# Kernel tuning notes

Measured on AMD Instinct MI355X. Metric: run time of the kernel, lower is better.

Reference implementation:

```python
import jax, jax.numpy as jnp
import numpy as np

JOINTS = 17
SKELETON = ((1, 2), (0, 1), (0, 2), (2, 4), (1, 3), (6, 8), (8, 10), (5, 7), (7, 9),
            (12, 14), (14, 16), (11, 13), (13, 15), (5, 6), (11, 12), (5, 11), (6, 12),
            (3, 5), (4, 6))
DIM = 512
HEADS = 8
HEAD_DIM = DIM // HEADS
SCALE = HEAD_DIM ** -0.5
ON = 64           # obj_emb seq len; HEADS*ON must equal 512 (size of W)
HIDDEN = 4 * DIM
BN_EPS = 1e-5
LN_EPS = 1e-5


def make_adj():
    a = np.eye(JOINTS, dtype=np.float32)
    for i, j in SKELETON:
        a[i, j] = 1.0
        a[j, i] = 1.0
    return jnp.asarray(a)


def layer_norm(x, w, b):
    mu = jnp.mean(x, axis=-1, keepdims=True)
    var = jnp.var(x, axis=-1, keepdims=True)
    return (x - mu) * jax.lax.rsqrt(var + LN_EPS) * w + b


def setup_inputs() -> dict:
    key = jax.random.key(0)
    ks = jax.random.split(key, 12)
    B = 2048
    inp = {
        "noise": jax.random.normal(ks[0], (B, JOINTS, DIM), jnp.float32),
        "obj_emb": jax.random.normal(ks[1], (B, ON, DIM), jnp.float32),
        "ln1_w": jnp.ones((DIM,), jnp.float32),
        "ln1_b": jnp.zeros((DIM,), jnp.float32),
        "ln2_w": jnp.ones((DIM,), jnp.float32),
        "ln2_b": jnp.zeros((DIM,), jnp.float32),
        "q_w": jax.random.normal(ks[2], (DIM, DIM), jnp.float32) * 0.02,
        "kv_w": jax.random.normal(ks[3], (2 * DIM, DIM), jnp.float32) * 0.02,
        "W": jax.random.normal(ks[4], (HEADS * ON, HEADS * ON), jnp.float32) * 0.001,
        "bn_g": jnp.ones((HEADS * ON,), jnp.float32),
        "bn_b": jnp.zeros((HEADS * ON,), jnp.float32),
        "proj_w": jax.random.normal(ks[5], (DIM, DIM), jnp.float32) * 0.02,
        "proj_b": jnp.zeros((DIM,), jnp.float32),
        "fc1_w": jax.random.normal(ks[6], (HIDDEN, DIM), jnp.float32) * 0.02,
        "fc1_b": jnp.zeros((HIDDEN,), jnp.float32),
        "fc2_w": jax.random.normal(ks[7], (DIM, HIDDEN), jnp.float32) * 0.02,
        "fc2_b": jnp.zeros((DIM,), jnp.float32),
    }
    return inp


def reference(noise, obj_emb, ln1_w, ln1_b, ln2_w, ln2_b, q_w, kv_w, W,
              bn_g, bn_b, proj_w, proj_b, fc1_w, fc1_b, fc2_w, fc2_b):
    B = noise.shape[0]
    adj = make_adj()

    # --- attention branch (norm1 applied to both inputs with same params) ---
    x1 = layer_norm(noise, ln1_w, ln1_b)          # [B,17,C]
    e1 = layer_norm(obj_emb, ln1_w, ln1_b)        # [B,64,C]

    q = (x1 @ q_w.T).reshape(B, JOINTS, HEADS, HEAD_DIM).transpose(0, 2, 1, 3)  # [B,H,17,hd]
    kv = (e1 @ kv_w.T).reshape(B, ON, 2, HEADS, HEAD_DIM).transpose(2, 0, 3, 1, 4)
    k, v = kv[0], kv[1]                            # [B,H,64,hd]

    attn = jnp.einsum('bhnd,bhmd->bhnm', q, k) * SCALE        # [B,H,17,64]
    attn = attn.transpose(0, 2, 1, 3).reshape(B, JOINTS, HEADS * ON)  # [B,17,512]
    attn = attn @ W                                            # [B,17,512]

    # BatchNorm1d (training mode): stats over B*17 rows, biased variance
    flat = attn.reshape(B * JOINTS, HEADS * ON)
    mu = jnp.mean(flat, axis=0)
    var = jnp.var(flat, axis=0)
    flat = (flat - mu) * jax.lax.rsqrt(var + BN_EPS) * bn_g + bn_b
    attn = flat.reshape(B, JOINTS, HEADS * ON)

    attn = jnp.einsum('ij,bjk->bik', adj, attn)               # adjacency bmm
    attn = attn.reshape(B, JOINTS, HEADS, ON).transpose(0, 2, 1, 3)  # [B,H,17,64]
    attn = jax.nn.softmax(attn, axis=-1)

    x = jnp.einsum('bhnm,bhmd->bhnd', attn, v)                # [B,H,17,hd]
    x = x.transpose(0, 2, 1, 3).reshape(B, JOINTS, DIM)
    x = x @ proj_w.T + proj_b

    x = noise + x

    # --- MLP branch ---
    y = layer_norm(x, ln2_w, ln2_b)
    y = jax.nn.gelu(y @ fc1_w.T + fc1_b, approximate=False)
    y = y @ fc2_w.T + fc2_b
    return x + y
```

## Files before the change

### kernel.cpp

```cpp
#include <hip/hip_runtime.h>
#include <math.h>

typedef unsigned short ushort_t;
typedef short short8 __attribute__((ext_vector_type(8)));
typedef float f32x4 __attribute__((ext_vector_type(4)));

#define MFMA16(a,b,c) __builtin_amdgcn_mfma_f32_16x16x32_bf16(a,b,c,0,0,0)

__device__ __forceinline__ ushort_t f2bf(float f){
  unsigned u = __builtin_bit_cast(unsigned, f);
  u += 0x7fffu + ((u >> 16) & 1u);
  return (ushort_t)(u >> 16);
}

__device__ __forceinline__ void gld16(const void* g, void* l){
  __builtin_amdgcn_global_load_lds(
      (const __attribute__((address_space(1))) void*)g,
      (__attribute__((address_space(3))) void*)l, 16, 0, 0);
}

__global__ __launch_bounds__(256)
void prep_weights(const float* __restrict__ q_w, const float* __restrict__ kv_w,
                  const float* __restrict__ proj_w, const float* __restrict__ fc1_w,
                  const float* __restrict__ fc2_w, const float* __restrict__ Wm,
                  const float* __restrict__ ln1w, const float* __restrict__ ln2w,
                  ushort_t* __restrict__ q_wb, ushort_t* __restrict__ kv_wb,
                  ushort_t* __restrict__ proj_wb, ushort_t* __restrict__ fc1_wb,
                  ushort_t* __restrict__ fc2_wb, ushort_t* __restrict__ Wt_b)
{
  int i = blockIdx.x*256 + threadIdx.x;
  if (i < 262144){
    q_wb[i] = f2bf(q_w[i] * ln1w[i & 511]);
  } else if (i < 786432){
    int j = i - 262144;
    kv_wb[j] = f2bf(kv_w[j] * ln1w[j & 511]);
  } else if (i < 1048576){
    int j = i - 786432;
    proj_wb[j] = f2bf(proj_w[j]);
  } else if (i < 2097152){
    int j = i - 1048576;
    fc1_wb[j] = f2bf(fc1_w[j] * ln2w[j & 511]);
  } else if (i < 3145728){
    int j = i - 2097152;
    fc2_wb[j] = f2bf(fc2_w[j]);
  } else if (i < 3407872){
    int j = i - 3145728;
    int n = j >> 9, k = j & 511;
    Wt_b[j] = f2bf(Wm[(k << 9) + n]);
  }
}

__global__ __launch_bounds__(64)
void prep_bias(const float* __restrict__ q_w, const float* __restrict__ kv_w,
               const float* __restrict__ fc1_w, const float* __restrict__ ln1b,
               const float* __restrict__ ln2b, const float* __restrict__ fc1_b,
               float* __restrict__ qbias, float* __restrict__ kvbias,
               float* __restrict__ fc1bias)
{
  int blk = blockIdx.x, lane = threadIdx.x;
  const float* w; const float* lnb; float* o; float base = 0.f; int n;
  if (blk < 512){ n = blk; w = q_w; lnb = ln1b; o = qbias; }
  else if (blk < 1536){ n = blk - 512; w = kv_w; lnb = ln1b; o = kvbias; }
  else { n = blk - 1536; w = fc1_w; lnb = ln2b; o = fc1bias; }
  float s = 0.f;
  for (int k = lane; k < 512; k += 64) s += w[(size_t)n*512 + k]*lnb[k];
  for (int m = 32; m; m >>= 1) s += __shfl_xor(s, m);
  if (lane == 0){
    if (blk >= 1536) base = fc1_b[n];
    o[n] = s + base;
  }
}

__global__ __launch_bounds__(256)
void lnorm(const float* __restrict__ X, ushort_t* __restrict__ O){
  int row = blockIdx.x*4 + (threadIdx.x >> 6);
  int lane = threadIdx.x & 63;
  const float4* p = (const float4*)(X + (size_t)row*512 + lane*8);
  float4 a = p[0], c = p[1];
  float s = a.x+a.y+a.z+a.w + c.x+c.y+c.z+c.w;
  float q = a.x*a.x+a.y*a.y+a.z*a.z+a.w*a.w + c.x*c.x+c.y*c.y+c.z*c.z+c.w*c.w;
  for (int m = 32; m; m >>= 1){ s += __shfl_xor(s, m); q += __shfl_xor(q, m); }
  float mn = s*(1.f/512.f);
  float rs = rsqrtf(q*(1.f/512.f) - mn*mn + 1e-5f);
  short8 pk;
  pk[0]=(short)f2bf((a.x-mn)*rs); pk[1]=(short)f2bf((a.y-mn)*rs);
  pk[2]=(short)f2bf((a.z-mn)*rs); pk[3]=(short)f2bf((a.w-mn)*rs);
  pk[4]=(short)f2bf((c.x-mn)*rs); pk[5]=(short)f2bf((c.y-mn)*rs);
  pk[6]=(short)f2bf((c.z-mn)*rs); pk[7]=(short)f2bf((c.w-mn)*rs);
  *(short8*)(O + (size_t)row*512 + lane*8) = pk;
}

template<int BN, int EPI>
__global__ __launch_bounds__(512, 4)
void gemm256(const ushort_t* __restrict__ A, const ushort_t* __restrict__ Bt,
             int M, int N, int K,
             const float* __restrict__ bias, const float* __restrict__ resid,
             void* __restrict__ out, void* __restrict__ out2)
{
  constexpr int NR    = BN / 64;
  constexpr int ASLOT = 256 * 32;
  constexpr int BSLOT = BN * 32;
  constexpr int SLOT  = ASLOT + BSLOT;
  __shared__ __align__(16) ushort_t lds[3 * SLOT];

  const int tid  = threadIdx.x;
  const int wave = tid >> 6, lane = tid & 63;
  const int wm   = wave >> 2, wn = wave & 3;
  const int l15  = lane & 15, lq = lane >> 4;

  const int nwg = gridDim.x;
  const int qc = nwg >> 3, rc = nwg & 7;
  const int xcd = blockIdx.x & 7, sl = blockIdx.x >> 3;
  const int bid = (xcd < rc ? xcd*(qc+1) : rc*(qc+1) + (xcd-rc)*qc) + sl;

  const int tiles_n = N / BN;
  const int tn = bid % tiles_n, tm = bid / tiles_n;
  const int tileM = tm * 256, tileN = tn * BN;

  const int gsw = (((tid & 3) - ((tid >> 3) & 3)) & 3) * 8;
  const int srow = tid >> 2;

  int offA[8], offB[NR];
#pragma unroll
  for (int mi = 0; mi < 8; mi++){
    int r = wm*128 + mi*16 + l15;
    offA[mi] = r*32 + (((lq + (r >> 1)) & 3) * 8);
  }
#pragma unroll
  for (int ni = 0; ni < NR; ni++){
    int r = wn*(BN/4) + ni*16 + l15;
    offB[ni] = ASLOT + r*32 + (((lq + (r >> 1)) & 3) * 8);
  }

  f32x4 acc[8][NR] = {};

  const int NT = K >> 5;

  auto stage = [&](int step, int slot){
    ushort_t* base = lds + slot * SLOT;
    const int k0 = step * 32 + gsw;
#pragma unroll
    for (int i = 0; i < 2; i++)
      gld16(A + (size_t)(tileM + i*128 + srow)*K + k0,
            base + i*4096 + wave*512);
#pragma unroll
    for (int i = 0; i < BN/128; i++)
      gld16(Bt + (size_t)(tileN + i*128 + srow)*K + k0,
            base + ASLOT + i*4096 + wave*512);
  };

  stage(0, 0);
  stage(1, 1);
  if constexpr (BN == 256) asm volatile("s_waitcnt vmcnt(4)" ::: "memory");
  else                     asm volatile("s_waitcnt vmcnt(3)" ::: "memory");
  __builtin_amdgcn_sched_barrier(0);
  __builtin_amdgcn_s_barrier();

  int rs = 0;
  for (int s = 0; s < NT; ++s){
    const ushort_t* sb = lds + rs * SLOT;
    short8 bfr[NR];
#pragma unroll
    for (int ni = 0; ni < NR; ni++)
      bfr[ni] = *(const short8*)(sb + offB[ni]);

    const bool more = (s + 2 < NT);
    if (more){
      int r2 = rs + 2; if (r2 >= 3) r2 -= 3;
      stage(s + 2, r2);
    }

    __builtin_amdgcn_s_setprio(1);
#pragma unroll
    for (int mi = 0; mi < 8; mi++){
      short8 af = *(const short8*)(sb + offA[mi]);
#pragma unroll
      for (int ni = 0; ni < NR; ni++)
        acc[mi][ni] = MFMA16(af, bfr[ni], acc[mi][ni]);
    }
    __builtin_amdgcn_s_setprio(0);

    if (more){
      if constexpr (BN == 256) asm volatile("s_waitcnt vmcnt(4)" ::: "memory");
      else                     asm volatile("s_waitcnt vmcnt(3)" ::: "memory");
    } else {
      asm volatile("s_waitcnt vmcnt(0)" ::: "memory");
    }
    __builtin_amdgcn_sched_barrier(0);
    __builtin_amdgcn_s_barrier();

    rs = (rs == 2) ? 0 : rs + 1;
  }

#pragma unroll
  for (int ni = 0; ni < NR; ni++){
    int col = tileN + wn*(BN/4) + ni*16 + l15;
    float bv = bias ? bias[col] : 0.f;
    float cs = 0.f, cq = 0.f;
#pragma unroll
    for (int mi = 0; mi < 8; mi++){
      f32x4 v = acc[mi][ni];
      int row0 = tileM + wm*128 + mi*16 + lq*4;
      if constexpr (EPI == 4){
        if (col < 512){
          for (int j = 0; j < 4; j++){
            size_t idx = (size_t)(row0 + j)*512 + col;
            ((ushort_t*)out)[idx] = f2bf(v[j] + bv);
          }
        } else {
          int hh = (col - 512) >> 6, dd = (col - 512) & 63;
          int bb = row0 >> 6, mm0 = row0 & 63;
          ushort_t pk[4];
          for (int j = 0; j < 4; j++) pk[j] = f2bf(v[j] + bv);
          *(uint2*)((ushort_t*)out2 + ((((size_t)bb*8 + hh)*64 + dd) << 6) + mm0) =
              *(const uint2*)pk;
        }
      } else {
        for (int j = 0; j < 4; j++){
          int row = row0 + j;
          size_t idx = (size_t)row*N + col;
          float x = v[j] + bv;
          if constexpr (EPI == 0) ((ushort_t*)out)[idx] = f2bf(x);
          else if constexpr (EPI == 1) ((float*)out)[idx] = x;
          else if constexpr (EPI == 2) ((float*)out)[idx] = x + resid[idx];
          else if constexpr (EPI == 3){
            float g = 0.5f*x*(1.f + erff(x*0.70710678118f));
            ((ushort_t*)out)[idx] = f2bf(g);
          }
          else if constexpr (EPI == 5){
            ((float*)out)[idx] = x;
            cs += x; cq += x*x;
          }
        }
      }
    }
    if constexpr (EPI == 5){
      cs += __shfl_xor(cs, 16); cs += __shfl_xor(cs, 32);
      cq += __shfl_xor(cq, 16); cq += __shfl_xor(cq, 32);
      if (lq == 0){
        float* sums = (float*)out2;
        atomicAdd(&sums[col], cs);
        atomicAdd(&sums[512 + col], cq);
      }
    }
  }
}

__global__ __launch_bounds__(256)
void qk_kernel(const ushort_t* __restrict__ Q, const ushort_t* __restrict__ Kb,
               ushort_t* __restrict__ S)
{
  int b = blockIdx.x;
  int wave = threadIdx.x >> 6, lane = threadIdx.x & 63;
  for (int h = wave; h < 8; h += 4){
    f32x4 acc[2][4] = {};
    for (int kk = 0; kk < 2; kk++){
      int kd = kk*32 + (lane >> 4)*8;
      short8 a[2], bb[4];
      for (int mi = 0; mi < 2; mi++){
        int n = mi*16 + (lane & 15); if (n > 16) n = 16;
        a[mi] = *(const short8*)&Q[((size_t)b*17 + n)*512 + h*64 + kd];
      }
      for (int ni = 0; ni < 4; ni++){
        int m = ni*16 + (lane & 15);
        bb[ni] = *(const short8*)&Kb[((size_t)b*64 + m)*512 + h*64 + kd];
      }
      for (int mi = 0; mi < 2; mi++)
        for (int ni = 0; ni < 4; ni++)
          acc[mi][ni] = MFMA16(a[mi], bb[ni], acc[mi][ni]);
    }
    for (int mi = 0; mi < 2; mi++)
      for (int ni = 0; ni < 4; ni++)
        for (int j = 0; j < 4; j++){
          int rr = mi*16 + (lane >> 4)*4 + j;
          if (rr < 17)
            S[((size_t)b*17 + rr)*512 + h*64 + ni*16 + (lane & 15)] =
                f2bf(acc[mi][ni][j]*0.125f);
        }
  }
}

__global__ __launch_bounds__(256)
void pv_kernel(const ushort_t* __restrict__ P, const ushort_t* __restrict__ Vt,
               ushort_t* __restrict__ X)
{
  int b = blockIdx.x;
  int wave = threadIdx.x >> 6, lane = threadIdx.x & 63;
  for (int h = wave; h < 8; h += 4){
    f32x4 acc[2][4] = {};
    for (int kk = 0; kk < 2; kk++){
      int km = kk*32 + (lane >> 4)*8;
      short8 a[2], bb[4];
      for (int mi = 0; mi < 2; mi++){
        int n = mi*16 + (lane & 15); if (n > 16) n = 16;
        a[mi] = *(const short8*)&P[((size_t)b*17 + n)*512 + h*64 + km];
      }
      for (int ni = 0; ni < 4; ni++){
        int d = ni*16 + (lane & 15);
        bb[ni] = *(const short8*)&Vt[(((size_t)b*8 + h)*64 + d)*64 + km];
      }
      for (int mi = 0; mi < 2; mi++)
        for (int ni = 0; ni < 4; ni++)
          acc[mi][ni] = MFMA16(a[mi], bb[ni], acc[mi][ni]);
    }
    for (int mi = 0; mi < 2; mi++)
      for (int ni = 0; ni < 4; ni++)
        for (int j = 0; j < 4; j++){
          int rr = mi*16 + (lane >> 4)*4 + j;
          if (rr < 17)
            X[((size_t)b*17 + rr)*512 + h*64 + ni*16 + (lane & 15)] =
                f2bf(acc[mi][ni][j]);
        }
  }
}

__global__ void bn_finalize(const float* __restrict__ sums, const float* __restrict__ g,
                            const float* __restrict__ b, float* __restrict__ scale,
                            float* __restrict__ shift, float invN){
  int c = blockIdx.x*256 + threadIdx.x;
  if (c < 512){
    float mean = sums[c]*invN;
    float var  = sums[512 + c]*invN - mean*mean;
    float sc = g[c]*rsqrtf(var + 1e-5f);
    scale[c] = sc; shift[c] = b[c] - mean*sc;
  }
}

__constant__ unsigned ADJM[17] = {
  0x7u, 0xFu, 0x17u, 0x2Au, 0x54u, 0x8E8u, 0x1170u, 0x2A0u, 0x540u,
  0x280u, 0x500u, 0x3820u, 0x5840u, 0xA800u, 0x15000u, 0xA000u, 0x14000u };

__global__ __launch_bounds__(256)
void bn_adj_softmax(const float* __restrict__ preBN, const float* __restrict__ scale,
                    const float* __restrict__ shift, ushort_t* __restrict__ Asm)
{
  __shared__ float yt[17*512];
  int b = blockIdx.x, tid = threadIdx.x;
  const float* src = preBN + (size_t)b*17*512;
  for (int i = tid; i < 17*512; i += 256){
    int c = i & 511;
    yt[i] = src[i]*scale[c] + shift[c];
  }
  __syncthreads();
  int qw = tid >> 4, l16 = tid & 15;
  for (int g = qw; g < 136; g += 16){
    int n = g >> 3, h = g & 7;
    float z[4];
    unsigned msk = ADJM[n];
    for (int u = 0; u < 4; u++){
      int c = h*64 + l16 + u*16;
      float sv = 0.f;
      unsigned mm = msk;
      while (mm){ int j = __ffs(mm) - 1; mm &= mm - 1; sv += yt[j*512 + c]; }
      z[u] = sv;
    }
    float mx = fmaxf(fmaxf(z[0], z[1]), fmaxf(z[2], z[3]));
    for (int m = 8; m; m >>= 1) mx = fmaxf(mx, __shfl_xor(mx, m, 16));
    float e0 = expf(z[0]-mx), e1 = expf(z[1]-mx), e2 = expf(z[2]-mx), e3 = expf(z[3]-mx);
    float ss = e0 + e1 + e2 + e3;
    for (int m = 8; m; m >>= 1) ss += __shfl_xor(ss, m, 16);
    float inv = 1.f/ss;
    size_t ob = ((size_t)b*17 + n)*512 + h*64 + l16;
    Asm[ob]      = f2bf(e0*inv);
    Asm[ob + 16] = f2bf(e1*inv);
    Asm[ob + 32] = f2bf(e2*inv);
    Asm[ob + 48] = f2bf(e3*inv);
  }
}

extern "C" void kernel_launch(void* const* d_in, const int* in_sizes, int n_in,
                              void* d_out, int out_size, void* d_ws, size_t ws_size,
                              hipStream_t stream)
{
  const float* noise  = (const float*)d_in[0];
  const float* obj    = (const float*)d_in[1];
  const float* ln1w   = (const float*)d_in[2];
  const float* ln1b   = (const float*)d_in[3];
  const float* ln2w   = (const float*)d_in[4];
  const float* ln2b   = (const float*)d_in[5];
  const float* q_w    = (const float*)d_in[6];
  const float* kv_w   = (const float*)d_in[7];
  const float* Wm     = (const float*)d_in[8];
  const float* bn_g   = (const float*)d_in[9];
  const float* bn_b   = (const float*)d_in[10];
  const float* proj_w = (const float*)d_in[11];
  const float* proj_b = (const float*)d_in[12];
  const float* fc1_w  = (const float*)d_in[13];
  const float* fc1_b  = (const float*)d_in[14];
  const float* fc2_w  = (const float*)d_in[15];
  const float* fc2_b  = (const float*)d_in[16];

  const int B  = in_sizes[0] / (17*512);
  const int M  = B*17;
  const int MO = B*64;

  const size_t MiB = 1ull << 20;
  char* ws = (char*)d_ws;

  ushort_t* q_wb    = (ushort_t*)(ws + 0*MiB);
  ushort_t* kv_wb   = (ushort_t*)(ws + 1*MiB);
  ushort_t* proj_wb = (ushort_t*)(ws + 2*MiB);
  ushort_t* fc1_wb  = (ushort_t*)(ws + 3*MiB);
  ushort_t* fc2_wb  = (ushort_t*)(ws + 5*MiB);
  ushort_t* Wt_b    = (ushort_t*)(ws + 7*MiB);
  float* qbias   = (float*)(ws + 7*MiB + 600*1024);
  float* kvbias  = qbias + 1024;
  float* fc1bias = kvbias + 1024;
  float* bnsum   = fc1bias + 2048;
  float* bnscale = bnsum + 1024;
  float* bnshift = bnscale + 512;

  char* R1 = ws + 8*MiB;
  char* R2 = ws + 136*MiB;
  char* R3 = ws + 264*MiB;

  ushort_t* e1b  = (ushort_t*)R1;
  ushort_t* Kb   = (ushort_t*)R2;
  ushort_t* Vtb  = (ushort_t*)R3;
  ushort_t* x1b  = (ushort_t*)R1;
  ushort_t* Qb   = (ushort_t*)(R1 + 35*MiB);
  ushort_t* Sb   = (ushort_t*)(R1 + 70*MiB);
  ushort_t* Asm  = (ushort_t*)R1;
  ushort_t* PVo  = (ushort_t*)(R1 + 35*MiB);
  float*    preBN = (float*)R2;
  float*    xres  = (float*)R2;
  ushort_t* yb   = (ushort_t*)(R2 + 69*MiB);
  ushort_t* h1   = (ushort_t*)(R2 + 104*MiB);
  float*    outp = (float*)d_out;

  hipMemsetAsync(bnsum, 0, 1024*4, stream);
  prep_weights<<<dim3(3407872/256), 256, 0, stream>>>(
      q_w, kv_w, proj_w, fc1_w, fc2_w, Wm, ln1w, ln2w,
      q_wb, kv_wb, proj_wb, fc1_wb, fc2_wb, Wt_b);
  prep_bias<<<dim3(3584), 64, 0, stream>>>(
      q_w, kv_w, fc1_w, ln1b, ln2b, fc1_b, qbias, kvbias, fc1bias);

  lnorm<<<dim3(MO/4), 256, 0, stream>>>(obj, e1b);
  gemm256<128,4><<<dim3((MO/256)*(1024/128)), 512, 0, stream>>>(
      e1b, kv_wb, MO, 1024, 512, kvbias, nullptr, Kb, Vtb);
  lnorm<<<dim3(M/4), 256, 0, stream>>>(noise, x1b);
  gemm256<128,0><<<dim3((M/256)*(512/128)), 512, 0, stream>>>(
      x1b, q_wb, M, 512, 512, qbias, nullptr, Qb, nullptr);
  qk_kernel<<<dim3(B), 256, 0, stream>>>(Qb, Kb, Sb);
  gemm256<128,5><<<dim3((M/256)*(512/128)), 512, 0, stream>>>(
      Sb, Wt_b, M, 512, 512, nullptr, nullptr, preBN, bnsum);
  bn_finalize<<<dim3(2), 256, 0, stream>>>(bnsum, bn_g, bn_b, bnscale, bnshift, 1.f/(float)M);
  bn_adj_softmax<<<dim3(B), 256, 0, stream>>>(preBN, bnscale, bnshift, Asm);
  pv_kernel<<<dim3(B), 256, 0, stream>>>(Asm, Vtb, PVo);
  gemm256<128,2><<<dim3((M/256)*(512/128)), 512, 0, stream>>>(
      PVo, proj_wb, M, 512, 512, proj_b, noise, xres, nullptr);

  lnorm<<<dim3(M/4), 256, 0, stream>>>(xres, yb);
  gemm256<128,3><<<dim3((M/256)*(2048/128)), 512, 0, stream>>>(
      yb, fc1_wb, M, 2048, 512, fc1bias, nullptr, h1, nullptr);
  gemm256<128,2><<<dim3((M/256)*(512/128)), 512, 0, stream>>>(
      h1, fc2_wb, M, 512, 2048, fc2_b, xres, outp, nullptr);
}
```

Baseline: 928.5 us.

## Replace GEMM with 256x256-tile, K=64, four-phase ping-pong pipelined kernel

Swaps the 256xBN triple-buffered GEMM for a 256x256 tile kernel with a 64-wide K step and double-buffered LDS (128KB). Each K iteration is split into four MFMA phases whose LDS fragment loads are interleaved with partial global-to-LDS prefetches for later steps, using an 8-way XOR swizzle. The aim is more reuse per tile and better overlap of global loads with MFMA work. In exchange it lowers occupancy to 2 blocks per CU and launches half as many tiles, so the small-N GEMMs (N=512, M≈35k) get fewer workgroups to spread across CUs.

```diff
diff --git a/kernel.cpp b/kernel.cpp
--- a/kernel.cpp
+++ b/kernel.cpp
@@ -90,18 +90,14 @@
   *(short8*)(O + (size_t)row*512 + lane*8) = pk;
 }
 
-template<int BN, int EPI>
-__global__ __launch_bounds__(512, 4)
-void gemm256(const ushort_t* __restrict__ A, const ushort_t* __restrict__ Bt,
-             int M, int N, int K,
-             const float* __restrict__ bias, const float* __restrict__ resid,
-             void* __restrict__ out, void* __restrict__ out2)
-{
-  constexpr int NR    = BN / 64;
-  constexpr int ASLOT = 256 * 32;
-  constexpr int BSLOT = BN * 32;
-  constexpr int SLOT  = ASLOT + BSLOT;
-  __shared__ __align__(16) ushort_t lds[3 * SLOT];
+template<int EPI>
+__global__ __launch_bounds__(512, 2)
+void gemm8p(const ushort_t* __restrict__ A, const ushort_t* __restrict__ Bt,
+            int M, int N, int K,
+            const float* __restrict__ bias, const float* __restrict__ resid,
+            void* __restrict__ out, void* __restrict__ out2)
+{
+  __shared__ __align__(16) ushort_t lds[65536];
 
   const int tid  = threadIdx.x;
   const int wave = tid >> 6, lane = tid & 63;
@@ -113,94 +109,157 @@
   const int xcd = blockIdx.x & 7, sl = blockIdx.x >> 3;
   const int bid = (xcd < rc ? xcd*(qc+1) : rc*(qc+1) + (xcd-rc)*qc) + sl;
 
-  const int tiles_n = N / BN;
+  const int tiles_n = N >> 8;
   const int tn = bid % tiles_n, tm = bid / tiles_n;
-  const int tileM = tm * 256, tileN = tn * BN;
-
-  const int gsw = (((tid & 3) - ((tid >> 3) & 3)) & 3) * 8;
-  const int srow = tid >> 2;
-
-  int offA[8], offB[NR];
-#pragma unroll
-  for (int mi = 0; mi < 8; mi++){
-    int r = wm*128 + mi*16 + l15;
-    offA[mi] = r*32 + (((lq + (r >> 1)) & 3) * 8);
-  }
-#pragma unroll
-  for (int ni = 0; ni < NR; ni++){
-    int r = wn*(BN/4) + ni*16 + l15;
-    offB[ni] = ASLOT + r*32 + (((lq + (r >> 1)) & 3) * 8);
-  }
-
-  f32x4 acc[8][NR] = {};
-
-  const int NT = K >> 5;
-
-  auto stage = [&](int step, int slot){
-    ushort_t* base = lds + slot * SLOT;
-    const int k0 = step * 32 + gsw;
-#pragma unroll
-    for (int i = 0; i < 2; i++)
-      gld16(A + (size_t)(tileM + i*128 + srow)*K + k0,
-            base + i*4096 + wave*512);
-#pragma unroll
-    for (int i = 0; i < BN/128; i++)
-      gld16(Bt + (size_t)(tileN + i*128 + srow)*K + k0,
-            base + ASLOT + i*4096 + wave*512);
+  const int tileM = tm*256, tileN = tn*256;
+
+  const int srow = tid >> 3;
+  const int gsw  = (((tid & 7) - (srow & 7)) & 7) * 8;
+  const ushort_t* Agl = A  + (size_t)(tileM + srow)*K + gsw;
+  const ushort_t* Bgl = Bt + (size_t)(tileN + srow)*K + gsw;
+
+  auto stageA = [&](int kt, int buf, int h){
+    ushort_t* d = lds + buf*32768 + h*8192 + tid*8;
+    const ushort_t* s = Agl + (size_t)(h*128)*K + kt*64;
+    gld16(s, d);
+    gld16(s + (size_t)64*K, d + 4096);
   };
-
-  stage(0, 0);
-  stage(1, 1);
-  if constexpr (BN == 256) asm volatile("s_waitcnt vmcnt(4)" ::: "memory");
-  else                     asm volatile("s_waitcnt vmcnt(3)" ::: "memory");
+  auto stageB = [&](int kt, int buf, int h){
+    ushort_t* d = lds + buf*32768 + 16384 + h*8192 + tid*8;
+    const ushort_t* s = Bgl + (size_t)(h*128)*K + kt*64;
+    gld16(s, d);
+    gld16(s + (size_t)64*K, d + 4096);
+  };
+
+  const int rbase = l15 * 64;
+  const int sk0 = (((lq    ) + (l15 & 7)) & 7) * 8;
+  const int sk1 = (((lq + 4) + (l15 & 7)) & 7) * 8;
+
+  f32x4 acc[8][4] = {};
+  short8 aR[4][2], b0R[2][2], b1R[2][2];
+
+  auto ldA = [&](const ushort_t* bb, int qm){
+#pragma unroll
+    for (int i = 0; i < 4; i++){
+      int ro = ((qm*4 + i)*2 + wm)*1024 + rbase;
+      aR[i][0] = *(const short8*)(bb + ro + sk0);
+      aR[i][1] = *(const short8*)(bb + ro + sk1);
+    }
+  };
+  auto ldB0 = [&](const ushort_t* bb){
+#pragma unroll
+    for (int j = 0; j < 2; j++){
+      int ro = 16384 + (j*4 + wn)*1024 + rbase;
+      b0R[j][0] = *(const short8*)(bb + ro + sk0);
+      b0R[j][1] = *(const short8*)(bb + ro + sk1);
+    }
+  };
+  auto ldB1 = [&](const ushort_t* bb){
+#pragma unroll
+    for (int j = 0; j < 2; j++){
+      int ro = 16384 + ((2 + j)*4 + wn)*1024 + rbase;
+      b1R[j][0] = *(const short8*)(bb + ro + sk0);
+      b1R[j][1] = *(const short8*)(bb + ro + sk1);
+    }
+  };
+
+  const int NT = K >> 6;
+
+  stageA(0, 0, 0);
+  stageB(0, 0, 0);
+  stageB(0, 0, 1);
+  stageA(0, 0, 1);
+  if (NT > 1){ stageA(1, 1, 0); stageB(1, 1, 1); stageA(1, 1, 1); }
+  asm volatile("s_waitcnt vmcnt(6)" ::: "memory");
   __builtin_amdgcn_sched_barrier(0);
   __builtin_amdgcn_s_barrier();
-
-  int rs = 0;
-  for (int s = 0; s < NT; ++s){
-    const ushort_t* sb = lds + rs * SLOT;
-    short8 bfr[NR];
-#pragma unroll
-    for (int ni = 0; ni < NR; ni++)
-      bfr[ni] = *(const short8*)(sb + offB[ni]);
-
-    const bool more = (s + 2 < NT);
-    if (more){
-      int r2 = rs + 2; if (r2 >= 3) r2 -= 3;
-      stage(s + 2, r2);
-    }
-
+  __builtin_amdgcn_sched_barrier(0);
+
+#define PHASE_SYNC(VMC)                                        \
+    asm volatile("s_waitcnt lgkmcnt(0)" ::: "memory");         \
+    __builtin_amdgcn_sched_barrier(0);                         \
+    asm volatile("s_waitcnt vmcnt(" VMC ")" ::: "memory");     \
+    __builtin_amdgcn_sched_barrier(0);                         \
+    __builtin_amdgcn_s_barrier();                              \
+    __builtin_amdgcn_sched_barrier(0);
+
+  for (int u = 0; u < NT; ++u){
+    const int buf = u & 1;
+    const ushort_t* bb = lds + buf*32768;
+
+    ldA(bb, 0); ldB0(bb);
+    if (u + 1 < NT) stageB(u+1, buf^1, 0);
+    PHASE_SYNC("6")
     __builtin_amdgcn_s_setprio(1);
 #pragma unroll
-    for (int mi = 0; mi < 8; mi++){
-      short8 af = *(const short8*)(sb + offA[mi]);
-#pragma unroll
-      for (int ni = 0; ni < NR; ni++)
-        acc[mi][ni] = MFMA16(af, bfr[ni], acc[mi][ni]);
-    }
+    for (int i = 0; i < 4; i++)
+#pragma unroll
+      for (int j = 0; j < 2; j++){
+        acc[i][j] = MFMA16(aR[i][0], b0R[j][0], acc[i][j]);
+        acc[i][j] = MFMA16(aR[i][1], b0R[j][1], acc[i][j]);
+      }
     __builtin_amdgcn_s_setprio(0);
-
-    if (more){
-      if constexpr (BN == 256) asm volatile("s_waitcnt vmcnt(4)" ::: "memory");
-      else                     asm volatile("s_waitcnt vmcnt(3)" ::: "memory");
+    __builtin_amdgcn_sched_barrier(0);
+
+    ldB1(bb);
+    if (u + 2 < NT) stageA(u+2, buf, 0);
+    PHASE_SYNC("6")
+    __builtin_amdgcn_s_setprio(1);
+#pragma unroll
+    for (int i = 0; i < 4; i++)
+#pragma unroll
+      for (int j = 0; j < 2; j++){
+        acc[i][2+j] = MFMA16(aR[i][0], b1R[j][0], acc[i][2+j]);
+        acc[i][2+j] = MFMA16(aR[i][1], b1R[j][1], acc[i][2+j]);
+      }
+    __builtin_amdgcn_s_setprio(0);
+    __builtin_amdgcn_sched_barrier(0);
+
+    ldA(bb, 1);
+    if (u + 2 < NT) stageB(u+2, buf, 1);
+    PHASE_SYNC("6")
+    __builtin_amdgcn_s_setprio(1);
+#pragma unroll
+    for (int i = 0; i < 4; i++)
+#pragma unroll
+      for (int j = 0; j < 2; j++){
+        acc[4+i][2+j] = MFMA16(aR[i][0], b1R[j][0], acc[4+i][2+j]);
+        acc[4+i][2+j] = MFMA16(aR[i][1], b1R[j][1], acc[4+i][2+j]);
+      }
+    __builtin_amdgcn_s_setprio(0);
+    __builtin_amdgcn_sched_barrier(0);
+
+    if (u + 2 < NT){
+      stageA(u+2, buf, 1);
+      asm volatile("s_waitcnt vmcnt(6)" ::: "memory");
     } else {
       asm volatile("s_waitcnt vmcnt(0)" ::: "memory");
     }
     __builtin_amdgcn_sched_barrier(0);
     __builtin_amdgcn_s_barrier();
-
-    rs = (rs == 2) ? 0 : rs + 1;
-  }
-
-#pragma unroll
-  for (int ni = 0; ni < NR; ni++){
-    int col = tileN + wn*(BN/4) + ni*16 + l15;
+    __builtin_amdgcn_sched_barrier(0);
+    __builtin_amdgcn_s_setprio(1);
+#pragma unroll
+    for (int i = 0; i < 4; i++)
+#pragma unroll
+      for (int j = 0; j < 2; j++){
+        acc[4+i][j] = MFMA16(aR[i][0], b0R[j][0], acc[4+i][j]);
+        acc[4+i][j] = MFMA16(aR[i][1], b0R[j][1], acc[4+i][j]);
+      }
+    __builtin_amdgcn_s_setprio(0);
+    __builtin_amdgcn_sched_barrier(0);
+  }
+#undef PHASE_SYNC
+
+#pragma unroll
+  for (int ni = 0; ni < 4; ni++){
+    int col = tileN + (ni*4 + wn)*16 + l15;
     float bv = bias ? bias[col] : 0.f;
     float cs = 0.f, cq = 0.f;
 #pragma unroll
     for (int mi = 0; mi < 8; mi++){
       f32x4 v = acc[mi][ni];
-      int row0 = tileM + wm*128 + mi*16 + lq*4;
+      int row0 = tileM + (mi*2 + wm)*16 + lq*4;
       if constexpr (EPI == 4){
         if (col < 512){
           for (int j = 0; j < 4; j++){
@@ -209,10 +268,10 @@
           }
         } else {
           int hh = (col - 512) >> 6, dd = (col - 512) & 63;
-          int bb = row0 >> 6, mm0 = row0 & 63;
+          int bb2 = row0 >> 6, mm0 = row0 & 63;
           ushort_t pk[4];
           for (int j = 0; j < 4; j++) pk[j] = f2bf(v[j] + bv);
-          *(uint2*)((ushort_t*)out2 + ((((size_t)bb*8 + hh)*64 + dd) << 6) + mm0) =
+          *(uint2*)((ushort_t*)out2 + ((((size_t)bb2*8 + hh)*64 + dd) << 6) + mm0) =
               *(const uint2*)pk;
         }
       } else {
@@ -436,23 +495,23 @@
       q_w, kv_w, fc1_w, ln1b, ln2b, fc1_b, qbias, kvbias, fc1bias);
 
   lnorm<<<dim3(MO/4), 256, 0, stream>>>(obj, e1b);
-  gemm256<128,4><<<dim3((MO/256)*(1024/128)), 512, 0, stream>>>(
+  gemm8p<4><<<dim3((MO/256)*(1024/256)), 512, 0, stream>>>(
       e1b, kv_wb, MO, 1024, 512, kvbias, nullptr, Kb, Vtb);
   lnorm<<<dim3(M/4), 256, 0, stream>>>(noise, x1b);
-  gemm256<128,0><<<dim3((M/256)*(512/128)), 512, 0, stream>>>(
+  gemm8p<0><<<dim3((M/256)*(512/256)), 512, 0, stream>>>(
       x1b, q_wb, M, 512, 512, qbias, nullptr, Qb, nullptr);
   qk_kernel<<<dim3(B), 256, 0, stream>>>(Qb, Kb, Sb);
-  gemm256<128,5><<<dim3((M/256)*(512/128)), 512, 0, stream>>>(
+  gemm8p<5><<<dim3((M/256)*(512/256)), 512, 0, stream>>>(
       Sb, Wt_b, M, 512, 512, nullptr, nullptr, preBN, bnsum);
   bn_finalize<<<dim3(2), 256, 0, stream>>>(bnsum, bn_g, bn_b, bnscale, bnshift, 1.f/(float)M);
   bn_adj_softmax<<<dim3(B), 256, 0, stream>>>(preBN, bnscale, bnshift, Asm);
   pv_kernel<<<dim3(B), 256, 0, stream>>>(Asm, Vtb, PVo);
-  gemm256<128,2><<<dim3((M/256)*(512/128)), 512, 0, stream>>>(
+  gemm8p<2><<<dim3((M/256)*(512/256)), 512, 0, stream>>>(
       PVo, proj_wb, M, 512, 512, proj_b, noise, xres, nullptr);
 
   lnorm<<<dim3(M/4), 256, 0, stream>>>(xres, yb);
-  gemm256<128,3><<<dim3((M/256)*(2048/128)), 512, 0, stream>>>(
+  gemm8p<3><<<dim3((M/256)*(2048/256)), 512, 0, stream>>>(
       yb, fc1_wb, M, 2048, 512, fc1bias, nullptr, h1, nullptr);
-  gemm256<128,2><<<dim3((M/256)*(512/128)), 512, 0, stream>>>(
+  gemm8p<2><<<dim3((M/256)*(512/256)), 512, 0, stream>>>(
       h1, fc2_wb, M, 512, 2048, fc2_b, xres, outp, nullptr);
 }
```

New measurement: 1.036 ms. 1.12x slower.

## Switch GEMMs to 256x256 tiles with B fragments loaded directly from global

Applied to the files above, without the earlier changes.

Replaces the templated 256xBN GEMM with a fixed 256x256-tile kernel. A is staged through triple-buffered LDS, while each wave loads its B fragments straight from global memory into double-buffered registers, with the K loop unrolled by two. This halves the number of workgroups and removes B from LDS traffic, aiming to improve reuse and free LDS bandwidth. The cost is lower occupancy (launch bounds 2), higher register pressure, fewer tiles for small GEMMs (e.g. 256 blocks for the N=512 GEMMs), and uncoalesced B loads whose latency the register double-buffering must hide.

```diff
diff --git a/kernel.cpp b/kernel.cpp
--- a/kernel.cpp
+++ b/kernel.cpp
@@ -90,18 +90,14 @@
   *(short8*)(O + (size_t)row*512 + lane*8) = pk;
 }
 
-template<int BN, int EPI>
-__global__ __launch_bounds__(512, 4)
-void gemm256(const ushort_t* __restrict__ A, const ushort_t* __restrict__ Bt,
+template<int EPI>
+__global__ __launch_bounds__(512, 2)
+void gemm_dg(const ushort_t* __restrict__ A, const ushort_t* __restrict__ Bt,
              int M, int N, int K,
              const float* __restrict__ bias, const float* __restrict__ resid,
              void* __restrict__ out, void* __restrict__ out2)
 {
-  constexpr int NR    = BN / 64;
-  constexpr int ASLOT = 256 * 32;
-  constexpr int BSLOT = BN * 32;
-  constexpr int SLOT  = ASLOT + BSLOT;
-  __shared__ __align__(16) ushort_t lds[3 * SLOT];
+  __shared__ __align__(16) ushort_t lds[3*8192];
 
   const int tid  = threadIdx.x;
   const int wave = tid >> 6, lane = tid & 63;
@@ -113,88 +109,91 @@
   const int xcd = blockIdx.x & 7, sl = blockIdx.x >> 3;
   const int bid = (xcd < rc ? xcd*(qc+1) : rc*(qc+1) + (xcd-rc)*qc) + sl;
 
-  const int tiles_n = N / BN;
+  const int tiles_n = N >> 8;
   const int tn = bid % tiles_n, tm = bid / tiles_n;
-  const int tileM = tm * 256, tileN = tn * BN;
-
-  const int gsw = (((tid & 3) - ((tid >> 3) & 3)) & 3) * 8;
-  const int srow = tid >> 2;
-
-  int offA[8], offB[NR];
+  const int tileM = tm*256, tileN = tn*256;
+
+  const int lr  = tid >> 2;
+  const int gA  = (((tid & 3) - lr - (lr >> 2)) & 3) * 8;
+  const ushort_t* AglStg = A + (size_t)(tileM + lr)*K + gA;
+  const int stgoff = tid*8;
+
+  const ushort_t* BglFrag = Bt + (size_t)(tileN + wn*64 + l15)*K + lq*8;
+
+  const int aoff = l15*32 + (((lq + l15 + (l15 >> 2)) & 3) * 8);
+
+  f32x4 acc[8][4] = {};
+  short8 aR[8], bE[4], bO[4];
+
+  const int NT = K >> 5;
+
+  {
+    ushort_t* d0 = lds + stgoff;
+    gld16(AglStg, d0);
+    gld16(AglStg + (size_t)128*K, d0 + 4096);
+    ushort_t* d1 = lds + 8192 + stgoff;
+    gld16(AglStg + 32, d1);
+    gld16(AglStg + (size_t)128*K + 32, d1 + 4096);
 #pragma unroll
-  for (int mi = 0; mi < 8; mi++){
-    int r = wm*128 + mi*16 + l15;
-    offA[mi] = r*32 + (((lq + (r >> 1)) & 3) * 8);
-  }
-#pragma unroll
-  for (int ni = 0; ni < NR; ni++){
-    int r = wn*(BN/4) + ni*16 + l15;
-    offB[ni] = ASLOT + r*32 + (((lq + (r >> 1)) & 3) * 8);
-  }
-
-  f32x4 acc[8][NR] = {};
-
-  const int NT = K >> 5;
-
-  auto stage = [&](int step, int slot){
-    ushort_t* base = lds + slot * SLOT;
-    const int k0 = step * 32 + gsw;
-#pragma unroll
-    for (int i = 0; i < 2; i++)
-      gld16(A + (size_t)(tileM + i*128 + srow)*K + k0,
-            base + i*4096 + wave*512);
-#pragma unroll
-    for (int i = 0; i < BN/128; i++)
-      gld16(Bt + (size_t)(tileN + i*128 + srow)*K + k0,
-            base + ASLOT + i*4096 + wave*512);
-  };
-
-  stage(0, 0);
-  stage(1, 1);
-  if constexpr (BN == 256) asm volatile("s_waitcnt vmcnt(4)" ::: "memory");
-  else                     asm volatile("s_waitcnt vmcnt(3)" ::: "memory");
-  __builtin_amdgcn_sched_barrier(0);
-  __builtin_amdgcn_s_barrier();
-
-  int rs = 0;
-  for (int s = 0; s < NT; ++s){
-    const ushort_t* sb = lds + rs * SLOT;
-    short8 bfr[NR];
-#pragma unroll
-    for (int ni = 0; ni < NR; ni++)
-      bfr[ni] = *(const short8*)(sb + offB[ni]);
-
-    const bool more = (s + 2 < NT);
-    if (more){
-      int r2 = rs + 2; if (r2 >= 3) r2 -= 3;
-      stage(s + 2, r2);
-    }
-
-    __builtin_amdgcn_s_setprio(1);
-#pragma unroll
-    for (int mi = 0; mi < 8; mi++){
-      short8 af = *(const short8*)(sb + offA[mi]);
-#pragma unroll
-      for (int ni = 0; ni < NR; ni++)
-        acc[mi][ni] = MFMA16(af, bfr[ni], acc[mi][ni]);
-    }
-    __builtin_amdgcn_s_setprio(0);
-
-    if (more){
-      if constexpr (BN == 256) asm volatile("s_waitcnt vmcnt(4)" ::: "memory");
-      else                     asm volatile("s_waitcnt vmcnt(3)" ::: "memory");
-    } else {
-      asm volatile("s_waitcnt vmcnt(0)" ::: "memory");
-    }
+    for (int ni = 0; ni < 4; ni++)
+      bE[ni] = *(const short8*)(BglFrag + (size_t)(ni*16)*K);
+    asm volatile("s_waitcnt vmcnt(6)" ::: "memory");
     __builtin_amdgcn_sched_barrier(0);
     __builtin_amdgcn_s_barrier();
-
-    rs = (rs == 2) ? 0 : rs + 1;
-  }
+    __builtin_amdgcn_sched_barrier(0);
+  }
+
+#define GTILE(U, BUSE, BLOAD, SLOTRD, SLOTSTG)                            \
+  {                                                                       \
+    const int u_ = (U);                                                   \
+    if (u_ + 1 < NT){                                                     \
+      const int kb = (u_ + 1) * 32;                                       \
+      _Pragma("unroll")                                                   \
+      for (int ni = 0; ni < 4; ni++)                                      \
+        BLOAD[ni] = *(const short8*)(BglFrag + (size_t)(ni*16)*K + kb);   \
+    }                                                                     \
+    if (u_ + 2 < NT){                                                     \
+      ushort_t* d = (SLOTSTG) + stgoff;                                   \
+      const ushort_t* s = AglStg + (u_ + 2)*32;                           \
+      gld16(s, d);                                                        \
+      gld16(s + (size_t)128*K, d + 4096);                                 \
+    }                                                                     \
+    { const ushort_t* rp = (SLOTRD) + wm*4096 + aoff;                     \
+      _Pragma("unroll")                                                   \
+      for (int mi = 0; mi < 8; mi++)                                      \
+        aR[mi] = *(const short8*)(rp + mi*512); }                         \
+    __builtin_amdgcn_s_setprio(1);                                        \
+    _Pragma("unroll")                                                     \
+    for (int mi = 0; mi < 8; mi++)                                        \
+      _Pragma("unroll")                                                   \
+      for (int ni = 0; ni < 4; ni++)                                      \
+        acc[mi][ni] = MFMA16(aR[mi], BUSE[ni], acc[mi][ni]);              \
+    __builtin_amdgcn_s_setprio(0);                                        \
+    if (u_ + 2 < NT){                                                     \
+      asm volatile("s_waitcnt vmcnt(6)" ::: "memory");                    \
+    } else if (u_ + 1 < NT){                                              \
+      asm volatile("s_waitcnt vmcnt(4)" ::: "memory");                    \
+    }                                                                     \
+    if (u_ + 1 < NT){                                                     \
+      __builtin_amdgcn_sched_barrier(0);                                  \
+      __builtin_amdgcn_s_barrier();                                       \
+      __builtin_amdgcn_sched_barrier(0);                                  \
+    }                                                                     \
+  }
+
+  int sl0 = 0;
+  for (int v = 0; v < NT; v += 2){
+    int sl1 = sl0 + 1; if (sl1 > 2) sl1 -= 3;
+    int sl2 = sl1 + 1; if (sl2 > 2) sl2 -= 3;
+    GTILE(v,     bE, bO, lds + sl0*8192, lds + sl2*8192);
+    GTILE(v + 1, bO, bE, lds + sl1*8192, lds + sl0*8192);
+    sl0 = sl2;
+  }
+#undef GTILE
 
 #pragma unroll
-  for (int ni = 0; ni < NR; ni++){
-    int col = tileN + wn*(BN/4) + ni*16 + l15;
+  for (int ni = 0; ni < 4; ni++){
+    int col = tileN + wn*64 + ni*16 + l15;
     float bv = bias ? bias[col] : 0.f;
     float cs = 0.f, cq = 0.f;
 #pragma unroll
@@ -209,10 +208,10 @@
           }
         } else {
           int hh = (col - 512) >> 6, dd = (col - 512) & 63;
-          int bb = row0 >> 6, mm0 = row0 & 63;
+          int bb2 = row0 >> 6, mm0 = row0 & 63;
           ushort_t pk[4];
           for (int j = 0; j < 4; j++) pk[j] = f2bf(v[j] + bv);
-          *(uint2*)((ushort_t*)out2 + ((((size_t)bb*8 + hh)*64 + dd) << 6) + mm0) =
+          *(uint2*)((ushort_t*)out2 + ((((size_t)bb2*8 + hh)*64 + dd) << 6) + mm0) =
               *(const uint2*)pk;
         }
       } else {
@@ -436,23 +435,23 @@
       q_w, kv_w, fc1_w, ln1b, ln2b, fc1_b, qbias, kvbias, fc1bias);
 
   lnorm<<<dim3(MO/4), 256, 0, stream>>>(obj, e1b);
-  gemm256<128,4><<<dim3((MO/256)*(1024/128)), 512, 0, stream>>>(
+  gemm_dg<4><<<dim3((MO/256)*(1024/256)), 512, 0, stream>>>(
       e1b, kv_wb, MO, 1024, 512, kvbias, nullptr, Kb, Vtb);
   lnorm<<<dim3(M/4), 256, 0, stream>>>(noise, x1b);
-  gemm256<128,0><<<dim3((M/256)*(512/128)), 512, 0, stream>>>(
+  gemm_dg<0><<<dim3((M/256)*(512/256)), 512, 0, stream>>>(
       x1b, q_wb, M, 512, 512, qbias, nullptr, Qb, nullptr);
   qk_kernel<<<dim3(B), 256, 0, stream>>>(Qb, Kb, Sb);
-  gemm256<128,5><<<dim3((M/256)*(512/128)), 512, 0, stream>>>(
+  gemm_dg<5><<<dim3((M/256)*(512/256)), 512, 0, stream>>>(
       Sb, Wt_b, M, 512, 512, nullptr, nullptr, preBN, bnsum);
   bn_finalize<<<dim3(2), 256, 0, stream>>>(bnsum, bn_g, bn_b, bnscale, bnshift, 1.f/(float)M);
   bn_adj_softmax<<<dim3(B), 256, 0, stream>>>(preBN, bnscale, bnshift, Asm);
   pv_kernel<<<dim3(B), 256, 0, stream>>>(Asm, Vtb, PVo);
-  gemm256<128,2><<<dim3((M/256)*(512/128)), 512, 0, stream>>>(
+  gemm_dg<2><<<dim3((M/256)*(512/256)), 512, 0, stream>>>(
       PVo, proj_wb, M, 512, 512, proj_b, noise, xres, nullptr);
 
   lnorm<<<dim3(M/4), 256, 0, stream>>>(xres, yb);
-  gemm256<128,3><<<dim3((M/256)*(2048/128)), 512, 0, stream>>>(
+  gemm_dg<3><<<dim3((M/256)*(2048/256)), 512, 0, stream>>>(
       yb, fc1_wb, M, 2048, 512, fc1bias, nullptr, h1, nullptr);
-  gemm256<128,2><<<dim3((M/256)*(512/128)), 512, 0, stream>>>(
+  gemm_dg<2><<<dim3((M/256)*(512/256)), 512, 0, stream>>>(
       h1, fc2_wb, M, 512, 2048, fc2_b, xres, outp, nullptr);
 }
```

After: 1.358 ms. +46.3%, slower.
